# Kernel tuning notes

Measured on AMD Instinct MI355X. Metric: run time of the kernel, lower is better.

## Reference

```python
import jax, jax.numpy as jnp
import numpy as np

N_ITER = 5  # from init_kwargs


def setup_inputs() -> dict:
    key = jax.random.key(0)
    k1, k2 = jax.random.split(key)
    K, F, B = 4, 513, 4000
    Xr = jax.random.normal(k1, (K, F, B), dtype=jnp.float32)
    Xi = jax.random.normal(k2, (K, F, B), dtype=jnp.float32)
    return {"Xr": Xr, "Xi": Xi}


def _auxiva(X):
    # X: complex64 (K, F, B)
    K, F, B = X.shape
    # XXh[i,j,f,b] = X[i,f,b] * conj(X[j,f,b])
    XXh = jnp.einsum('ifb,jfb->ijfb', X, X.conj())
    Wh = jnp.tile(jnp.eye(K, dtype=X.dtype)[None], (F, 1, 1))  # (F, K, K)
    for _ in range(N_ITER):
        Y = jnp.einsum('fsc,cfb->sfb', Wh, X)          # demix: (K, F, B)
        r = jnp.linalg.norm(Y, axis=1)                  # (K, B), real
        phi = 1.0 / (2.0 * r)                           # laplace contrast
        # V[k,i,j,f] = mean_b phi[k,b] * XXh[i,j,f,b]  (avoid (K,K,K,F,B) blowup)
        V = jnp.einsum('kb,ijfb->kijf', phi.astype(X.dtype), XXh) / B
        for k in range(K):                              # sequential IP updates
            M = jnp.einsum('fik,kjf->fij', Wh, V[k])    # (F, K, K)
            w = jnp.linalg.inv(M)[:, :, k].conj()       # (F, K)
            denom = jnp.sqrt(jnp.einsum('fc,ckf,fk->f', w, V[k], w.conj()))
            Wh = Wh.at[:, k, :].set(w / denom[:, None])
    Y = jnp.einsum('fsc,cfb->sfb', Wh, X)
    scale = jnp.linalg.inv(Wh)[:, :, 0]                 # projection back: (F, K)
    return jnp.einsum('sfb,fs->sfb', Y, scale)


def reference(Xr, Xi):
    X = (Xr + 1j * Xi).astype(jnp.complex64)
    return _auxiva(X)
```

## Files before the change

kernel.cpp:

```cpp
#include <hip/hip_runtime.h>
#include <hip/hip_bf16.h>
#include <math.h>

#define K 4
#define F 513
#define B 4000
#define NIT 5
#define FB (F*B)
#define KB (K*B)
#define DFC 4
#define NDF 129
#define NBC 4
#define BCH (B/NBC)

__device__ float2 g_Wh[F*16];
__device__ float2 g_V[64*F];
__device__ float2 g_scale[F*4];
__device__ float  g_r2p[NDF*KB];
__device__ float4 g_phiT[B];

struct cd { double re, im; };
__device__ inline cd mkcd(double r, double i){ cd z; z.re=r; z.im=i; return z; }
__device__ inline cd cmul(cd a, cd b){ return mkcd(a.re*b.re - a.im*b.im, a.re*b.im + a.im*b.re); }
__device__ inline cd cadd(cd a, cd b){ return mkcd(a.re+b.re, a.im+b.im); }
__device__ inline cd csub(cd a, cd b){ return mkcd(a.re-b.re, a.im-b.im); }
__device__ inline cd conj_(cd a){ return mkcd(a.re, -a.im); }
__device__ inline cd cdiv(cd a, cd b){
  double d = b.re*b.re + b.im*b.im;
  return mkcd((a.re*b.re + a.im*b.im)/d, (a.im*b.re - a.re*b.im)/d);
}

__device__ inline void invcol4(const cd M[4][4], int kk, cd x[4]){
  int r0 = (kk==0)?1:0;
  int r1 = (kk<=1)?2:1;
  int r2 = (kk<=2)?3:2;
  cd cof[4];
  #pragma unroll
  for (int i=0;i<4;++i){
    int c0 = (i==0)?1:0;
    int c1 = (i<=1)?2:1;
    int c2 = (i<=2)?3:2;
    cd m = cadd(csub(cmul(M[r0][c0], csub(cmul(M[r1][c1],M[r2][c2]), cmul(M[r1][c2],M[r2][c1]))),
                     cmul(M[r0][c1], csub(cmul(M[r1][c0],M[r2][c2]), cmul(M[r1][c2],M[r2][c0])))),
                cmul(M[r0][c2], csub(cmul(M[r1][c0],M[r2][c1]), cmul(M[r1][c1],M[r2][c0]))));
    if ((kk+i)&1) m = mkcd(-m.re,-m.im);
    cof[i] = m;
  }
  cd det = mkcd(0.0,0.0);
  #pragma unroll
  for (int i=0;i<4;++i) det = cadd(det, cmul(M[kk][i], cof[i]));
  cd idet = cdiv(mkcd(1.0,0.0), det);
  #pragma unroll
  for (int i=0;i<4;++i) x[i] = cmul(cof[i], idet);
}


__global__ __launch_bounds__(256) void demix_part_kernel(
    const float* __restrict__ Xr, const float* __restrict__ Xi, int it0){
  int t = blockIdx.x*blockDim.x + threadIdx.x;
  if (t >= B/2) return;
  int b = 2*t;
  int y = blockIdx.y;
  float acc0[K], acc1[K];
  #pragma unroll
  for (int s=0;s<K;++s){ acc0[s]=0.0f; acc1[s]=0.0f; }

  auto body = [&](int f){
    float2 xr[K], xi[K];
    #pragma unroll
    for (int c=0;c<K;++c){
      int idx = c*FB + f*B + b;
      xr[c] = *reinterpret_cast<const float2*>(Xr + idx);
      xi[c] = *reinterpret_cast<const float2*>(Xi + idx);
    }
    if (it0){
      #pragma unroll
      for (int s=0;s<K;++s){
        acc0[s] += xr[s].x*xr[s].x + xi[s].x*xi[s].x;
        acc1[s] += xr[s].y*xr[s].y + xi[s].y*xi[s].y;
      }
    } else {
      const float2* w = g_Wh + f*16;
      #pragma unroll
      for (int s=0;s<K;++s){
        float yr0=0.0f, yi0=0.0f, yr1=0.0f, yi1=0.0f;
        #pragma unroll
        for (int c=0;c<K;++c){
          float2 ww = w[s*4+c];
          yr0 += ww.x*xr[c].x - ww.y*xi[c].x;
          yi0 += ww.x*xi[c].x + ww.y*xr[c].x;
          yr1 += ww.x*xr[c].y - ww.y*xi[c].y;
          yi1 += ww.x*xi[c].y + ww.y*xr[c].y;
        }
        acc0[s] += yr0*yr0 + yi0*yi0;
        acc1[s] += yr1*yr1 + yi1*yi1;
      }
    }
  };

  if (y < 128){
    int f0 = y*DFC;
    #pragma unroll
    for (int ff=0; ff<DFC; ++ff) body(f0+ff);
  } else {
    body(512);
  }
  #pragma unroll
  for (int s=0;s<K;++s)
    *reinterpret_cast<float2*>(g_r2p + y*KB + s*B + b) = make_float2(acc0[s], acc1[s]);
}

__global__ __launch_bounds__(256) void phi_kernel(){
  int b = blockIdx.x*blockDim.x + threadIdx.x;
  int k = blockIdx.y;
  int g = (blockIdx.y*gridDim.x + blockIdx.x)*256 + threadIdx.x;
  float* vz = reinterpret_cast<float*>(g_V);
  for (int j=g; j<64*F*2; j+=16384) vz[j] = 0.0f;
  if (b >= B) return;
  float s = 0.0f;
  #pragma unroll 8
  for (int y=0; y<NDF; ++y) s += g_r2p[y*KB + k*B + b];
  reinterpret_cast<float*>(g_phiT)[b*4 + k] = 0.5f / sqrtf(s);
}

__global__ __launch_bounds__(256, 3) void v_kernel(
    const float* __restrict__ Xr, const float* __restrict__ Xi){
  int f = blockIdx.x;
  int y = blockIdx.y;
  int tid = threadIdx.x;
  float acc[64];
  #pragma unroll
  for (int q=0;q<64;++q) acc[q]=0.0f;

  if (tid < BCH/4){
    int b = y*BCH + 4*tid;
    float4 ph[4];
    #pragma unroll
    for (int u=0;u<4;++u) ph[u] = g_phiT[b+u];
    float2 xr[K][2], xi[K][2];
    #pragma unroll
    for (int c=0;c<K;++c){
      int idx = c*FB + f*B + b;
      xr[c][0] = *reinterpret_cast<const float2*>(Xr + idx);
      xr[c][1] = *reinterpret_cast<const float2*>(Xr + idx + 2);
      xi[c][0] = *reinterpret_cast<const float2*>(Xi + idx);
      xi[c][1] = *reinterpret_cast<const float2*>(Xi + idx + 2);
    }
    #pragma unroll
    for (int u=0;u<4;++u){
      const int h = u >> 1;
      float vr[K], vi[K], pk[K];
      #pragma unroll
      for (int c=0;c<K;++c){
        vr[c] = (u&1) ? xr[c][h].y : xr[c][h].x;
        vi[c] = (u&1) ? xi[c][h].y : xi[c][h].x;
      }
      pk[0]=ph[u].x; pk[1]=ph[u].y; pk[2]=ph[u].z; pk[3]=ph[u].w;
      float p[16];
      #pragma unroll
      for (int i=0;i<4;++i) p[i] = vr[i]*vr[i] + vi[i]*vi[i];
      int s = 4;
      #pragma unroll
      for (int i=0;i<4;++i){
        #pragma unroll
        for (int j=i+1;j<4;++j){
          p[s++] = vr[i]*vr[j] + vi[i]*vi[j];
          p[s++] = vi[i]*vr[j] - vr[i]*vi[j];
        }
      }
      #pragma unroll
      for (int k=0;k<K;++k){
        #pragma unroll
        for (int q=0;q<16;++q) acc[k*16+q] += pk[k]*p[q];
      }
    }
  }

  int lane = tid & 63, wave = tid >> 6;
  #pragma unroll
  for (int d=0; d<6; ++d){
    const int sh = 1<<d;
    const bool hi = (lane & sh) != 0;
    #pragma unroll
    for (int m=0; m<(32>>d); ++m){
      float keep = hi ? acc[2*m+1] : acc[2*m];
      float send = hi ? acc[2*m]   : acc[2*m+1];
      acc[m] = keep + __shfl_xor(send, sh);
    }
  }

  __shared__ float part[4*64];
  __shared__ float red[64];
  part[wave*64 + lane] = acc[0];
  __syncthreads();
  if (tid < 64){
    red[tid] = (part[tid] + part[64+tid] + part[128+tid] + part[192+tid]) * (1.0f/B);
  }
  __syncthreads();
  if (tid < 64){
    int k = tid >> 4, ij = tid & 15, i = ij >> 2, j = ij & 3;
    float re, im;
    if (i == j){ re = red[k*16 + i]; im = 0.0f; }
    else {
      int a = min(i,j), c2 = max(i,j);
      int pidx = (a==0) ? (c2-1) : ((a==1) ? (c2+1) : 5);
      re = red[k*16 + 4 + 2*pidx];
      im = red[k*16 + 5 + 2*pidx];
      if (i > j) im = -im;
    }
    float* dst = reinterpret_cast<float*>(g_V) + ((unsigned)tid*F + f)*2;
    atomicAdd(dst,   re);
    atomicAdd(dst+1, im);
  }
}

__global__ __launch_bounds__(64, 1) void update_kernel(int it0, int do_scale){
  int f = blockIdx.x*blockDim.x + threadIdx.x;
  if (f >= F) return;

  float2 Vf[64];
  #pragma unroll
  for (int q=0;q<64;++q) Vf[q] = g_V[q*F + f];

  cd W[4][4];
  if (it0){
    #pragma unroll
    for (int s=0;s<4;++s)
      #pragma unroll
      for (int c=0;c<4;++c) W[s][c] = mkcd(s==c ? 1.0 : 0.0, 0.0);
  } else {
    #pragma unroll
    for (int s=0;s<4;++s)
      #pragma unroll
      for (int c=0;c<4;++c){ float2 w = g_Wh[f*16+s*4+c]; W[s][c] = mkcd((double)w.x,(double)w.y); }
  }

  #pragma unroll
  for (int k=0;k<4;++k){
    cd Vk[4][4];
    #pragma unroll
    for (int i=0;i<4;++i)
      #pragma unroll
      for (int j=0;j<4;++j){
        float2 vv = Vf[(k*4+i)*4+j];
        Vk[i][j] = mkcd((double)vv.x,(double)vv.y);
      }
    cd M[4][4];
    #pragma unroll
    for (int i=0;i<4;++i)
      #pragma unroll
      for (int j=0;j<4;++j){
        cd s = mkcd(0.0,0.0);
        #pragma unroll
        for (int c=0;c<4;++c) s = cadd(s, cmul(W[i][c], Vk[c][j]));
        M[i][j] = s;
      }
    cd x[4];
    invcol4(M, k, x);
    cd w[4];
    #pragma unroll
    for (int c=0;c<4;++c) w[c] = conj_(x[c]);
    double dre = 0.0;
    #pragma unroll
    for (int j=0;j<4;++j){
      cd tj = mkcd(0.0,0.0);
      #pragma unroll
      for (int c=0;c<4;++c) tj = cadd(tj, cmul(w[c], Vk[c][j]));
      dre += tj.re*w[j].re + tj.im*w[j].im;
    }
    double inv_denom = rsqrt(dre > 0.0 ? dre : 1e-300);
    #pragma unroll
    for (int c=0;c<4;++c) W[k][c] = mkcd(w[c].re*inv_denom, w[c].im*inv_denom);
  }
  #pragma unroll
  for (int s=0;s<4;++s)
    #pragma unroll
    for (int c=0;c<4;++c) g_Wh[f*16+s*4+c] = make_float2((float)W[s][c].re, (float)W[s][c].im);

  if (do_scale){
    cd x[4];
    invcol4(W, 0, x);
    #pragma unroll
    for (int s=0;s<4;++s) g_scale[f*4+s] = make_float2((float)x[s].re, (float)x[s].im);
  }
}

__global__ __launch_bounds__(256) void final_kernel(
    const float* __restrict__ Xr, const float* __restrict__ Xi,
    __hip_bfloat162* __restrict__ out){
  int t = blockIdx.x*blockDim.x + threadIdx.x;
  if (t >= B/2) return;
  int b = 2*t;
  int y = blockIdx.y;

  auto body = [&](int f){
    float2 xr[K], xi[K];
    #pragma unroll
    for (int c=0;c<K;++c){
      int idx = c*FB + f*B + b;
      xr[c] = *reinterpret_cast<const float2*>(Xr + idx);
      xi[c] = *reinterpret_cast<const float2*>(Xi + idx);
    }
    const float2* w = g_Wh + f*16;
    #pragma unroll
    for (int s=0;s<K;++s){
      float yr0=0.0f, yi0=0.0f, yr1=0.0f, yi1=0.0f;
      #pragma unroll
      for (int c=0;c<K;++c){
        float2 ww = w[s*4+c];
        yr0 += ww.x*xr[c].x - ww.y*xi[c].x;
        yi0 += ww.x*xi[c].x + ww.y*xr[c].x;
        yr1 += ww.x*xr[c].y - ww.y*xi[c].y;
        yi1 += ww.x*xi[c].y + ww.y*xr[c].y;
      }
      float2 sc = g_scale[f*4+s];
      union { __hip_bfloat162 h2[2]; uint2 u; } uu;
      uu.h2[0].x = __float2bfloat16(yr0*sc.x - yi0*sc.y);
      uu.h2[0].y = __float2bfloat16(yr0*sc.y + yi0*sc.x);
      uu.h2[1].x = __float2bfloat16(yr1*sc.x - yi1*sc.y);
      uu.h2[1].y = __float2bfloat16(yr1*sc.y + yi1*sc.x);
      *reinterpret_cast<uint2*>(out + s*FB + f*B + b) = uu.u;
    }
  };

  if (y < 128){
    int f0 = y*DFC;
    #pragma unroll
    for (int ff=0; ff<DFC; ++ff) body(f0+ff);
  } else {
    body(512);
  }
}

extern "C" void kernel_launch(void* const* d_in, const int* in_sizes, int n_in,
                              void* d_out, int out_size, void* d_ws, size_t ws_size,
                              hipStream_t stream){
  const float* Xr = (const float*)d_in[1];
  const float* Xi = (const float*)d_in[0];
  __hip_bfloat162* out = (__hip_bfloat162*)d_out;

  dim3 gD((B/2 + 255)/256, NDF);
  dim3 gP((B + 255)/256, K);
  dim3 gV(F, NBC);
  for (int it=0; it<NIT; ++it){
    demix_part_kernel<<<gD, 256, 0, stream>>>(Xr, Xi, it == 0 ? 1 : 0);
    phi_kernel<<<gP, 256, 0, stream>>>();
    v_kernel<<<gV, 256, 0, stream>>>(Xr, Xi);
    update_kernel<<<(F + 63)/64, 64, 0, stream>>>(it == 0 ? 1 : 0, it == NIT-1 ? 1 : 0);
  }
  final_kernel<<<gD, 256, 0, stream>>>(Xr, Xi, out);
}
```

Measured before the change: 381.0 us.

## Split V accumulation across waves per source and store compact Hermitian V

The weighted-covariance kernel now gives each of the four waves in a block one source k, so each thread keeps 16 accumulators instead of 64, and the grid uses eight batch chunks per frequency instead of four. The cross-lane reduction is shorter and there is no shared-memory stage. V is stored in compact real form: 16 floats per source, holding the diagonal plus the upper-triangle real and imaginary parts. The update kernel rebuilds the Hermitian matrix from these, which halves the atomics and the memory traffic. The cost is that each wave reloads the same X values (four times in total), and more blocks issue atomics.

```diff
diff --git a/kernel.cpp b/kernel.cpp
--- a/kernel.cpp
+++ b/kernel.cpp
@@ -10,14 +10,14 @@
 #define KB (K*B)
 #define DFC 4
 #define NDF 129
-#define NBC 4
+#define NBC 8
 #define BCH (B/NBC)
 
 __device__ float2 g_Wh[F*16];
-__device__ float2 g_V[64*F];
+__device__ float  g_Vk[64*F];
 __device__ float2 g_scale[F*4];
 __device__ float  g_r2p[NDF*KB];
-__device__ float4 g_phiT[B];
+__device__ float  g_phi[KB];
 
 struct cd { double re, im; };
 __device__ inline cd mkcd(double r, double i){ cd z; z.re=r; z.im=i; return z; }
@@ -111,116 +111,101 @@
 }
 
 __global__ __launch_bounds__(256) void phi_kernel(){
-  int b = blockIdx.x*blockDim.x + threadIdx.x;
-  int k = blockIdx.y;
-  int g = (blockIdx.y*gridDim.x + blockIdx.x)*256 + threadIdx.x;
-  float* vz = reinterpret_cast<float*>(g_V);
-  for (int j=g; j<64*F*2; j+=16384) vz[j] = 0.0f;
-  if (b >= B) return;
+  int t = blockIdx.x*blockDim.x + threadIdx.x;
+  if (t < 64*F) g_Vk[t] = 0.0f;
+  if (t >= KB) return;
   float s = 0.0f;
   #pragma unroll 8
-  for (int y=0; y<NDF; ++y) s += g_r2p[y*KB + k*B + b];
-  reinterpret_cast<float*>(g_phiT)[b*4 + k] = 0.5f / sqrtf(s);
-}
-
-__global__ __launch_bounds__(256, 3) void v_kernel(
+  for (int y=0; y<NDF; ++y) s += g_r2p[y*KB + t];
+  g_phi[t] = 0.5f / sqrtf(s);
+}
+
+__global__ __launch_bounds__(256, 6) void v_kernel(
     const float* __restrict__ Xr, const float* __restrict__ Xi){
-  int f = blockIdx.x;
-  int y = blockIdx.y;
-  int tid = threadIdx.x;
-  float acc[64];
-  #pragma unroll
-  for (int q=0;q<64;++q) acc[q]=0.0f;
-
-  if (tid < BCH/4){
-    int b = y*BCH + 4*tid;
-    float4 ph[4];
-    #pragma unroll
-    for (int u=0;u<4;++u) ph[u] = g_phiT[b+u];
-    float2 xr[K][2], xi[K][2];
-    #pragma unroll
-    for (int c=0;c<K;++c){
-      int idx = c*FB + f*B + b;
-      xr[c][0] = *reinterpret_cast<const float2*>(Xr + idx);
-      xr[c][1] = *reinterpret_cast<const float2*>(Xr + idx + 2);
-      xi[c][0] = *reinterpret_cast<const float2*>(Xi + idx);
-      xi[c][1] = *reinterpret_cast<const float2*>(Xi + idx + 2);
-    }
-    #pragma unroll
-    for (int u=0;u<4;++u){
-      const int h = u >> 1;
-      float vr[K], vi[K], pk[K];
+  const int f = blockIdx.x;
+  const int y = blockIdx.y;
+  const int tid = threadIdx.x;
+  const int k = tid >> 6;
+  const int lane = tid & 63;
+
+  float acc[16];
+  #pragma unroll
+  for (int q=0;q<16;++q) acc[q]=0.0f;
+
+  const int b0 = y*BCH;
+  #pragma unroll
+  for (int i=0;i<4;++i){
+    int pidx = lane + 64*i;
+    if (pidx < BCH/2){
+      int b = b0 + 2*pidx;
+      float2 ph = *reinterpret_cast<const float2*>(g_phi + k*B + b);
+      float2 xr[K], xi[K];
       #pragma unroll
       for (int c=0;c<K;++c){
-        vr[c] = (u&1) ? xr[c][h].y : xr[c][h].x;
-        vi[c] = (u&1) ? xi[c][h].y : xi[c][h].x;
-      }
-      pk[0]=ph[u].x; pk[1]=ph[u].y; pk[2]=ph[u].z; pk[3]=ph[u].w;
-      float p[16];
-      #pragma unroll
-      for (int i=0;i<4;++i) p[i] = vr[i]*vr[i] + vi[i]*vi[i];
-      int s = 4;
-      #pragma unroll
-      for (int i=0;i<4;++i){
-        #pragma unroll
-        for (int j=i+1;j<4;++j){
-          p[s++] = vr[i]*vr[j] + vi[i]*vi[j];
-          p[s++] = vi[i]*vr[j] - vr[i]*vi[j];
+        int idx = c*FB + f*B + b;
+        xr[c] = *reinterpret_cast<const float2*>(Xr + idx);
+        xi[c] = *reinterpret_cast<const float2*>(Xi + idx);
+      }
+      {
+        float p[16];
+        #pragma unroll
+        for (int a=0;a<4;++a) p[a] = xr[a].x*xr[a].x + xi[a].x*xi[a].x;
+        int s = 4;
+        #pragma unroll
+        for (int a=0;a<4;++a){
+          #pragma unroll
+          for (int j=a+1;j<4;++j){
+            p[s++] = xr[a].x*xr[j].x + xi[a].x*xi[j].x;
+            p[s++] = xi[a].x*xr[j].x - xr[a].x*xi[j].x;
+          }
         }
-      }
-      #pragma unroll
-      for (int k=0;k<K;++k){
-        #pragma unroll
-        for (int q=0;q<16;++q) acc[k*16+q] += pk[k]*p[q];
-      }
-    }
-  }
-
-  int lane = tid & 63, wave = tid >> 6;
-  #pragma unroll
-  for (int d=0; d<6; ++d){
+        #pragma unroll
+        for (int q=0;q<16;++q) acc[q] += ph.x*p[q];
+      }
+      {
+        float p[16];
+        #pragma unroll
+        for (int a=0;a<4;++a) p[a] = xr[a].y*xr[a].y + xi[a].y*xi[a].y;
+        int s = 4;
+        #pragma unroll
+        for (int a=0;a<4;++a){
+          #pragma unroll
+          for (int j=a+1;j<4;++j){
+            p[s++] = xr[a].y*xr[j].y + xi[a].y*xi[j].y;
+            p[s++] = xi[a].y*xr[j].y - xr[a].y*xi[j].y;
+          }
+        }
+        #pragma unroll
+        for (int q=0;q<16;++q) acc[q] += ph.y*p[q];
+      }
+    }
+  }
+
+  #pragma unroll
+  for (int d=0; d<4; ++d){
     const int sh = 1<<d;
     const bool hi = (lane & sh) != 0;
     #pragma unroll
-    for (int m=0; m<(32>>d); ++m){
+    for (int m=0; m<(8>>d); ++m){
       float keep = hi ? acc[2*m+1] : acc[2*m];
       float send = hi ? acc[2*m]   : acc[2*m+1];
       acc[m] = keep + __shfl_xor(send, sh);
     }
   }
-
-  __shared__ float part[4*64];
-  __shared__ float red[64];
-  part[wave*64 + lane] = acc[0];
-  __syncthreads();
-  if (tid < 64){
-    red[tid] = (part[tid] + part[64+tid] + part[128+tid] + part[192+tid]) * (1.0f/B);
-  }
-  __syncthreads();
-  if (tid < 64){
-    int k = tid >> 4, ij = tid & 15, i = ij >> 2, j = ij & 3;
-    float re, im;
-    if (i == j){ re = red[k*16 + i]; im = 0.0f; }
-    else {
-      int a = min(i,j), c2 = max(i,j);
-      int pidx = (a==0) ? (c2-1) : ((a==1) ? (c2+1) : 5);
-      re = red[k*16 + 4 + 2*pidx];
-      im = red[k*16 + 5 + 2*pidx];
-      if (i > j) im = -im;
-    }
-    float* dst = reinterpret_cast<float*>(g_V) + ((unsigned)tid*F + f)*2;
-    atomicAdd(dst,   re);
-    atomicAdd(dst+1, im);
-  }
+  acc[0] += __shfl_xor(acc[0], 16);
+  acc[0] += __shfl_xor(acc[0], 32);
+
+  if (lane < 16)
+    atomicAdd(&g_Vk[(k*16 + lane)*F + f], acc[0] * (1.0f/B));
 }
 
 __global__ __launch_bounds__(64, 1) void update_kernel(int it0, int do_scale){
   int f = blockIdx.x*blockDim.x + threadIdx.x;
   if (f >= F) return;
 
-  float2 Vf[64];
-  #pragma unroll
-  for (int q=0;q<64;++q) Vf[q] = g_V[q*F + f];
+  float Vf[64];
+  #pragma unroll
+  for (int q=0;q<64;++q) Vf[q] = g_Vk[q*F + f];
 
   cd W[4][4];
   if (it0){
@@ -237,13 +222,20 @@
 
   #pragma unroll
   for (int k=0;k<4;++k){
+    const float* vk = Vf + k*16;
     cd Vk[4][4];
     #pragma unroll
     for (int i=0;i<4;++i)
       #pragma unroll
       for (int j=0;j<4;++j){
-        float2 vv = Vf[(k*4+i)*4+j];
-        Vk[i][j] = mkcd((double)vv.x,(double)vv.y);
+        if (i == j) Vk[i][j] = mkcd((double)vk[i], 0.0);
+        else {
+          int a = min(i,j), c2 = max(i,j);
+          int pidx = (a==0) ? (c2-1) : ((a==1) ? (c2+1) : 5);
+          double re = (double)vk[4 + 2*pidx];
+          double im = (double)vk[5 + 2*pidx];
+          Vk[i][j] = mkcd(re, (i > j) ? -im : im);
+        }
       }
     cd M[4][4];
     #pragma unroll
@@ -340,11 +332,10 @@
   __hip_bfloat162* out = (__hip_bfloat162*)d_out;
 
   dim3 gD((B/2 + 255)/256, NDF);
-  dim3 gP((B + 255)/256, K);
   dim3 gV(F, NBC);
   for (int it=0; it<NIT; ++it){
     demix_part_kernel<<<gD, 256, 0, stream>>>(Xr, Xi, it == 0 ? 1 : 0);
-    phi_kernel<<<gP, 256, 0, stream>>>();
+    phi_kernel<<<NDF, 256, 0, stream>>>();
     v_kernel<<<gV, 256, 0, stream>>>(Xr, Xi);
     update_kernel<<<(F + 63)/64, 64, 0, stream>>>(it == 0 ? 1 : 0, it == NIT-1 ? 1 : 0);
   }
```

Result: no change. 382.0 us (+0.3%).
